# Kernel optimization log

Measured on AMD Instinct MI355X. Metric: run time of the kernel, lower is better.

The kernel has to match this reference:

```python
import jax, jax.numpy as jnp
import numpy as np


def mesa_head(xh, yh, qh, lam):
    # xh = per-head 'inputs' (v_proj output), yh = 'targets' (k_proj output),
    # qh = queries; all [T, d]. lam is this head's scalar lambda.
    T, d = xh.shape
    init_inv = jnp.eye(d, dtype=xh.dtype) * lam

    def step(inv, tok):
        x_t, q_t = tok
        Hx = inv @ x_t                      # [d]   (cur_inverse @ x)
        xH = x_t @ inv                      # [d]   (x^T @ cur_inverse)
        denom = 1.0 + x_t @ Hx              # scalar: forward=1 + x^T H x
        new_inv = inv - jnp.outer(Hx, xH) / denom   # Sherman-Morrison rank-1 update
        return new_inv, new_inv @ q_t       # pred_t = S_t @ q_t

    _, preds = jax.lax.scan(step, init_inv, (xh, qh))  # preds: [T, d]

    # scaled_dot_product_attention(preds, xh, yh) with masked=True,
    # use_softmax=False, normalization=False: tril-masked linear attention.
    logits = preds @ xh.T                               # [T, T]
    mask = jnp.tril(jnp.ones((T, T), dtype=bool))
    logits = jnp.where(mask, logits, jnp.zeros((), dtype=logits.dtype))
    return logits @ yh                                  # [T, d]


def reference(x, Wq, Wk, Wv, Wo, lambdas):
    B, T, E = x.shape
    H = lambdas.shape[0]
    d = Wq.shape[1] // H
    q = (x @ Wq).reshape(B, T, H, d)   # query_heads
    k = (x @ Wk).reshape(B, T, H, d)   # target_heads
    v = (x @ Wv).reshape(B, T, H, d)   # input_heads
    # Original call: mesa(input_heads, target_heads, query_heads, lambdas, norm)
    over_batch = jax.vmap(mesa_head, in_axes=(0, 0, 0, None))
    over_heads = jax.vmap(over_batch, in_axes=(2, 2, 2, 0), out_axes=-1)
    mesa_out = over_heads(v, k, q, lambdas)             # [B, T, d, H]
    # Faithful to original: reshape combines (d, H) in that order before o_proj.
    out = mesa_out.reshape(B, T, H * d) @ Wo            # [B, T, E]
    return out


def setup_inputs() -> dict:
    key = jax.random.key(0)
    ks = jax.random.split(key, 6)
    B, T, E, H, d = 2, 1024, 512, 8, 64
    s_in = 1.0 / np.sqrt(E).astype(np.float32)
    s_out = 1.0 / np.sqrt(H * d).astype(np.float32)
    return {
        "x": jax.random.normal(ks[0], (B, T, E), dtype=jnp.float32),
        "Wq": jax.random.normal(ks[1], (E, H * d), dtype=jnp.float32) * s_in,
        "Wk": jax.random.normal(ks[2], (E, H * d), dtype=jnp.float32) * s_in,
        "Wv": jax.random.normal(ks[3], (E, H * d), dtype=jnp.float32) * s_in,
        "Wo": jax.random.normal(ks[4], (H * d, E), dtype=jnp.float32) * s_out,
        "lambdas": jnp.ones((H,), dtype=jnp.float32),
    }
```

## Files before the change

### kernel.cpp

```cpp
#include <hip/hip_runtime.h>

#define T_SEQ 1024
#define DH 64
#define NH 8
#define NB 2
#define EMB 512
#define CS 32
#define NCH 32
#define ACH 16
#define NCHAIN 16

typedef __attribute__((ext_vector_type(8))) short bf16x8;
typedef __attribute__((ext_vector_type(4))) float f32x4;

__device__ __forceinline__ int swz4(int r, int c4) {
    return r * 16 + ((c4 ^ (r >> 2)) & 15);
}

__device__ __forceinline__ void fma4(float4& o, float s, const float4& b) {
    o.x += s * b.x; o.y += s * b.y; o.z += s * b.z; o.w += s * b.w;
}

__device__ __forceinline__ ushort f2bf(float f) {
    unsigned u = __float_as_uint(f);
    return (ushort)((u + 0x7FFFu + ((u >> 16) & 1u)) >> 16);
}
__device__ __forceinline__ float bf2f(ushort h) {
    return __uint_as_float(((unsigned)h) << 16);
}
__device__ __forceinline__ void split2(float f, ushort& hi, ushort& lo) {
    hi = f2bf(f);
    lo = f2bf(f - bf2f(hi));
}

__global__ __launch_bounds__(256) void prep_qkv(
    const float* __restrict__ x, const float* __restrict__ W0,
    const float* __restrict__ W1, const float* __restrict__ W2,
    ushort* __restrict__ x_hi, ushort* __restrict__ x_lo,
    ushort* __restrict__ Wt_hi, ushort* __restrict__ Wt_lo) {
    int zz = blockIdx.z;
    int t = threadIdx.x;
    __shared__ float T[64][65];
    if (zz < 3) {
        const float* W = (zz == 0) ? W0 : (zz == 1) ? W1 : W2;
        ushort* hi = Wt_hi + (size_t)zz * 262144;
        ushort* lo = Wt_lo + (size_t)zz * 262144;
        int kk0 = blockIdx.x * 64, n0 = blockIdx.y * 64;
#pragma unroll
        for (int i = 0; i < 4; ++i) {
            int rl = i * 16 + (t >> 4);
            float4 vv = *(const float4*)&W[(size_t)(kk0 + rl) * 512 + n0 + (t & 15) * 4];
            T[rl][(t & 15) * 4 + 0] = vv.x;
            T[rl][(t & 15) * 4 + 1] = vv.y;
            T[rl][(t & 15) * 4 + 2] = vv.z;
            T[rl][(t & 15) * 4 + 3] = vv.w;
        }
        __syncthreads();
        int nl = t >> 2, kl = (t & 3) * 16;
#pragma unroll
        for (int j4 = 0; j4 < 4; ++j4) {
            ushort4 h4, l4;
            split2(T[kl + j4 * 4 + 0][nl], h4.x, l4.x);
            split2(T[kl + j4 * 4 + 1][nl], h4.y, l4.y);
            split2(T[kl + j4 * 4 + 2][nl], h4.z, l4.z);
            split2(T[kl + j4 * 4 + 3][nl], h4.w, l4.w);
            size_t dst = (size_t)(n0 + nl) * 512 + kk0 + kl + j4 * 4;
            *(ushort4*)&hi[dst] = h4;
            *(ushort4*)&lo[dst] = l4;
        }
    } else {
        int bid = blockIdx.y * 8 + blockIdx.x;
        const float4* in = (const float4*)x;
        ushort4* hi = (ushort4*)x_hi;
        ushort4* lo = (ushort4*)x_lo;
#pragma unroll
        for (int i = 0; i < 16; ++i) {
            int id = (bid * 16 + i) * 256 + t;
            float4 xv = in[id];
            ushort4 h, l;
            split2(xv.x, h.x, l.x);
            split2(xv.y, h.y, l.y);
            split2(xv.z, h.z, l.z);
            split2(xv.w, h.w, l.w);
            hi[id] = h;
            lo[id] = l;
        }
    }
}

template <int MODE>
__global__ __launch_bounds__(256) void mfma_gemm(
    const ushort* __restrict__ Ahi, const ushort* __restrict__ Alo,
    const ushort* __restrict__ Bth, const ushort* __restrict__ Btl,
    float* __restrict__ o0, float* __restrict__ o1, float* __restrict__ o2) {
    int bm = blockIdx.x, bn = blockIdx.y, zz = blockIdx.z;
    const ushort* Bh = Bth + (size_t)zz * 262144;
    const ushort* Bl = Btl + (size_t)zz * 262144;
    float* out = (MODE == 0) ? ((zz == 0) ? o0 : (zz == 1) ? o1 : o2) : o0;

    __shared__ ushort Ash[128 * 40];
    __shared__ ushort Asl[128 * 40];
    __shared__ ushort Bsh[64 * 40];
    __shared__ ushort Bsl[64 * 40];

    int tid = threadIdx.x;
    int lane = tid & 63, wid = tid >> 6;
    int wm = wid >> 1, wn = wid & 1;
    int fr = lane & 15, fk = (lane >> 4) * 8;
    int sr = tid >> 2, sc = (tid & 3) * 8;

    f32x4 zero = {0.f, 0.f, 0.f, 0.f};
    f32x4 acc[4][2];
#pragma unroll
    for (int f = 0; f < 4; ++f)
#pragma unroll
        for (int g = 0; g < 2; ++g) acc[f][g] = zero;

    const ushort* gAh = Ahi + (size_t)(bm * 128 + sr) * 512 + sc;
    const ushort* gAl = Alo + (size_t)(bm * 128 + sr) * 512 + sc;
    const ushort* gBh = Bh + (size_t)(bn * 64 + sr) * 512 + sc;
    const ushort* gBl = Bl + (size_t)(bn * 64 + sr) * 512 + sc;

    for (int k0 = 0; k0 < 512; k0 += 32) {
        uint4 a0 = *(const uint4*)(gAh + k0);
        uint4 a1 = *(const uint4*)(gAh + 64 * 512 + k0);
        uint4 a2 = *(const uint4*)(gAl + k0);
        uint4 a3 = *(const uint4*)(gAl + 64 * 512 + k0);
        uint4 b0 = *(const uint4*)(gBh + k0);
        uint4 b1 = *(const uint4*)(gBl + k0);
        __syncthreads();
        *(uint4*)&Ash[sr * 40 + sc] = a0;
        *(uint4*)&Ash[(sr + 64) * 40 + sc] = a1;
        *(uint4*)&Asl[sr * 40 + sc] = a2;
        *(uint4*)&Asl[(sr + 64) * 40 + sc] = a3;
        *(uint4*)&Bsh[sr * 40 + sc] = b0;
        *(uint4*)&Bsl[sr * 40 + sc] = b1;
        __syncthreads();
        bf16x8 ah[4], al[4], bh[2], blo[2];
#pragma unroll
        for (int f = 0; f < 4; ++f) {
            int r = wm * 64 + f * 16 + fr;
            ah[f] = *(const bf16x8*)&Ash[r * 40 + fk];
            al[f] = *(const bf16x8*)&Asl[r * 40 + fk];
        }
#pragma unroll
        for (int g = 0; g < 2; ++g) {
            int r = wn * 32 + g * 16 + fr;
            bh[g] = *(const bf16x8*)&Bsh[r * 40 + fk];
            blo[g] = *(const bf16x8*)&Bsl[r * 40 + fk];
        }
#pragma unroll
        for (int f = 0; f < 4; ++f)
#pragma unroll
            for (int g = 0; g < 2; ++g) {
                acc[f][g] = __builtin_amdgcn_mfma_f32_16x16x32_bf16(
                    ah[f], bh[g], acc[f][g], 0, 0, 0);
                acc[f][g] = __builtin_amdgcn_mfma_f32_16x16x32_bf16(
                    ah[f], blo[g], acc[f][g], 0, 0, 0);
                acc[f][g] = __builtin_amdgcn_mfma_f32_16x16x32_bf16(
                    al[f], bh[g], acc[f][g], 0, 0, 0);
            }
    }

    int rbase = (lane >> 4) * 4;
#pragma unroll
    for (int f = 0; f < 4; ++f)
#pragma unroll
        for (int g = 0; g < 2; ++g)
#pragma unroll
            for (int j = 0; j < 4; ++j) {
                int m = bm * 128 + wm * 64 + f * 16 + rbase + j;
                int n = bn * 64 + wn * 32 + g * 16 + (lane & 15);
                float val = acc[f][g][j];
                if (MODE == 0) {
                    int b = m >> 10, tt = m & 1023;
                    int h = n >> 6, d = n & 63;
                    out[(((size_t)(b * 8 + h) * 1024 + tt) << 6) + d] = val;
                } else {
                    out[(size_t)m * 512 + n] = val;
                }
            }
}

__global__ __launch_bounds__(256) void gram_kernel(
    const float* __restrict__ v, float* __restrict__ g) {
    int chain = blockIdx.x, chunk = blockIdx.y;
    const float* X = v + ((size_t)chain * T_SEQ + chunk * CS) * DH;
    __shared__ float Xs[CS * 64];
    int tid = threadIdx.x;
#pragma unroll
    for (int i = 0; i < (CS * 16) / 256; ++i)
        ((float4*)Xs)[i * 256 + tid] = ((const float4*)X)[i * 256 + tid];
    __syncthreads();

    int tx = tid & 15, ty = tid >> 4;
    float acc[4][4];
#pragma unroll
    for (int i = 0; i < 4; ++i)
#pragma unroll
        for (int j = 0; j < 4; ++j) acc[i][j] = 0.f;

#pragma unroll 4
    for (int t = 0; t < CS; ++t) {
        float a_[4], b_[4];
#pragma unroll
        for (int i = 0; i < 4; ++i) a_[i] = Xs[t * 64 + ty * 4 + i];
#pragma unroll
        for (int j = 0; j < 4; ++j) b_[j] = Xs[t * 64 + tx * 4 + j];
#pragma unroll
        for (int i = 0; i < 4; ++i)
#pragma unroll
            for (int j = 0; j < 4; ++j) acc[i][j] += a_[i] * b_[j];
    }

    float* gp = g + ((size_t)chain * NCH + chunk) * 4096;
#pragma unroll
    for (int i = 0; i < 4; ++i)
        *(float4*)(gp + (ty * 4 + i) * 64 + tx * 4) =
            make_float4(acc[i][0], acc[i][1], acc[i][2], acc[i][3]);
}

__global__ __launch_bounds__(256) void prefix_kernel(float* __restrict__ g) {
    int gid = blockIdx.x * 256 + threadIdx.x;
    int chain = gid >> 12, elem = gid & 4095;
    float* p = g + (size_t)chain * NCH * 4096 + elem;
    float vals[NCH];
#pragma unroll
    for (int c = 0; c < NCH; ++c) vals[c] = p[(size_t)c * 4096];
    float run = 0.f;
#pragma unroll
    for (int c = 0; c < NCH; ++c) {
        float t = vals[c];
        vals[c] = run;
        run += t;
    }
#pragma unroll
    for (int c = 0; c < NCH; ++c) p[(size_t)c * 4096] = vals[c];
}

__global__ __launch_bounds__(256) void invscan(
    const float* __restrict__ g, const float* __restrict__ v,
    const float* __restrict__ q, const float* __restrict__ lambdas,
    float* __restrict__ preds) {
    int blk = blockIdx.x;
    int chain = blk >> 5, chunk = blk & 31;
    int tid = threadIdx.x;
    int row = tid >> 2, ch = tid & 3, wav = tid >> 6;
    float lam = lambdas[chain & (NH - 1)];

    __shared__ float rbuf[2][64];
    __shared__ float sbuf[2][64];
    __shared__ float Xs[CS * 64];
    __shared__ float Qs[CS * 64];
    __shared__ float Po[CS * 64];
    __shared__ float red[2][6][4];

    float m[16];
    {
        const float4* gp = (const float4*)(g + ((size_t)chain * NCH + chunk) * 4096);
#pragma unroll
        for (int i = 0; i < 4; ++i) {
            float4 t4 = gp[row * 16 + ch * 4 + i];
            m[i * 4 + 0] = t4.x; m[i * 4 + 1] = t4.y;
            m[i * 4 + 2] = t4.z; m[i * 4 + 3] = t4.w;
        }
    }
#pragma unroll
    for (int i = 0; i < 16; ++i)
        if (ch * 16 + i == row) m[i] += lam;

    const float4* vb = (const float4*)(v + ((size_t)chain * T_SEQ + chunk * CS) * DH);
    const float4* qb = (const float4*)(q + ((size_t)chain * T_SEQ + chunk * CS) * DH);
    ((float4*)Xs)[tid] = vb[tid];
    ((float4*)Xs)[256 + tid] = vb[256 + tid];
    ((float4*)Qs)[tid] = qb[tid];
    ((float4*)Qs)[256 + tid] = qb[256 + tid];

    if (row == 0) {
#pragma unroll
        for (int i = 0; i < 4; ++i)
            ((float4*)rbuf[0])[ch * 4 + i] =
                make_float4(m[i * 4], m[i * 4 + 1], m[i * 4 + 2], m[i * 4 + 3]);
    }
    if (row == 1) {
#pragma unroll
        for (int i = 0; i < 4; ++i)
            ((float4*)sbuf[0])[ch * 4 + i] =
                make_float4(m[i * 4], m[i * 4 + 1], m[i * 4 + 2], m[i * 4 + 3]);
    }
    __syncthreads();

#pragma unroll
    for (int pp = 0; pp < 32; ++pp) {
        const int p = 2 * pp;
        const float* rb = rbuf[pp & 1];
        const float* sb = sbuf[pp & 1];
        float r_[16], s_[16];
#pragma unroll
        for (int i = 0; i < 4; ++i) {
            float4 t4 = ((const float4*)rb)[ch * 4 + i];
            r_[i * 4] = t4.x; r_[i * 4 + 1] = t4.y;
            r_[i * 4 + 2] = t4.z; r_[i * 4 + 3] = t4.w;
            float4 u4 = ((const float4*)sb)[ch * 4 + i];
            s_[i * 4] = u4.x; s_[i * 4 + 1] = u4.y;
            s_[i * 4 + 2] = u4.z; s_[i * 4 + 3] = u4.w;
        }
        float rp = rb[p], rp2 = rb[p + 1], sp2 = sb[p + 1];
        float gr = rb[row], gs = sb[row];
        float i1 = 1.f / rp;
        float al = rp2 * i1;
        float i2 = 1.f / (sp2 - al * rp2);
        float c0, ca, cb;
        if (row == p) {
            c0 = 0.f; ca = i1 + al * al * i2; cb = -al * i2;
        } else if (row == p + 1) {
            c0 = 0.f; ca = -al * i2; cb = i2;
        } else {
            float b2 = (gs - al * gr) * i2;
            c0 = 1.f; ca = al * b2 - gr * i1; cb = -b2;
        }
#pragma unroll
        for (int i = 0; i < 16; ++i) m[i] = c0 * m[i] + ca * r_[i] + cb * s_[i];
        if (ch == (p >> 4)) {
            m[p & 15] = -ca;
            m[(p & 15) + 1] = -cb;
        }
        if (pp < 31) {
            if (row == p + 2) {
#pragma unroll
                for (int i = 0; i < 4; ++i)
                    ((float4*)rbuf[(pp + 1) & 1])[ch * 4 + i] =
                        make_float4(m[i * 4], m[i * 4 + 1], m[i * 4 + 2], m[i * 4 + 3]);
            }
            if (row == p + 3) {
#pragma unroll
                for (int i = 0; i < 4; ++i)
                    ((float4*)sbuf[(pp + 1) & 1])[ch * 4 + i] =
                        make_float4(m[i * 4], m[i * 4 + 1], m[i * 4 + 2], m[i * 4 + 3]);
            }
        }
        __syncthreads();
    }

#pragma unroll
    for (int tp = 0; tp < 16; ++tp) {
        const int ta = 2 * tp, tb2 = 2 * tp + 1;
        const int par = tp & 1;
        float pu = 0.f, pw = 0.f, pza = 0.f, pzb = 0.f;
#pragma unroll
        for (int i = 0; i < 4; ++i) {
            float4 xa = ((const float4*)(Xs + ta * 64))[ch * 4 + i];
            float4 xb = ((const float4*)(Xs + tb2 * 64))[ch * 4 + i];
            float4 qa = ((const float4*)(Qs + ta * 64))[ch * 4 + i];
            float4 q4 = ((const float4*)(Qs + tb2 * 64))[ch * 4 + i];
            pu += m[i * 4] * xa.x + m[i * 4 + 1] * xa.y + m[i * 4 + 2] * xa.z + m[i * 4 + 3] * xa.w;
            pw += m[i * 4] * xb.x + m[i * 4 + 1] * xb.y + m[i * 4 + 2] * xb.z + m[i * 4 + 3] * xb.w;
            pza += m[i * 4] * qa.x + m[i * 4 + 1] * qa.y + m[i * 4 + 2] * qa.z + m[i * 4 + 3] * qa.w;
            pzb += m[i * 4] * q4.x + m[i * 4 + 1] * q4.y + m[i * 4 + 2] * q4.z + m[i * 4 + 3] * q4.w;
        }
        pu += __shfl_xor(pu, 1); pu += __shfl_xor(pu, 2);
        pw += __shfl_xor(pw, 1); pw += __shfl_xor(pw, 2);
        pza += __shfl_xor(pza, 1); pza += __shfl_xor(pza, 2);
        pzb += __shfl_xor(pzb, 1); pzb += __shfl_xor(pzb, 2);
        float u = -pu, w = -pw, za = -pza, zb = -pzb;
        if (ch == 0) rbuf[par][row] = u;
        if (ch == 1) sbuf[par][row] = w;
        float a_ = Xs[ta * 64 + row], b_ = Xs[tb2 * 64 + row];
        float qa_ = Qs[ta * 64 + row], qb_ = Qs[tb2 * 64 + row];
        float d0 = a_ * u, d1 = b_ * u, d2 = b_ * w;
        float d3 = qa_ * u, d4 = qb_ * u, d5 = qb_ * w;
#pragma unroll
        for (int off = 32; off; off >>= 1) {
            d0 += __shfl_xor(d0, off); d1 += __shfl_xor(d1, off);
            d2 += __shfl_xor(d2, off); d3 += __shfl_xor(d3, off);
            d4 += __shfl_xor(d4, off); d5 += __shfl_xor(d5, off);
        }
        if ((tid & 63) == 0) {
            red[par][0][wav] = d0; red[par][1][wav] = d1; red[par][2][wav] = d2;
            red[par][3][wav] = d3; red[par][4][wav] = d4; red[par][5][wav] = d5;
        }
        __syncthreads();
        float saa = 0.25f * (red[par][0][0] + red[par][0][1] + red[par][0][2] + red[par][0][3]);
        float sab = 0.25f * (red[par][1][0] + red[par][1][1] + red[par][1][2] + red[par][1][3]);
        float sbb = 0.25f * (red[par][2][0] + red[par][2][1] + red[par][2][2] + red[par][2][3]);
        float c1  = 0.25f * (red[par][3][0] + red[par][3][1] + red[par][3][2] + red[par][3][3]);
        float c2  = 0.25f * (red[par][4][0] + red[par][4][1] + red[par][4][2] + red[par][4][3]);
        float c3  = 0.25f * (red[par][5][0] + red[par][5][1] + red[par][5][2] + red[par][5][3]);
        float k1 = 1.f / (1.f + saa);
        float al2 = sab * k1;
        float k2 = 1.f / (1.f + sbb - sab * al2);
        float vr = w - al2 * u;
        if (ch == 0) Po[ta * 64 + row] = za - (c1 * k1) * u;
        if (ch == 1) Po[tb2 * 64 + row] = zb - (c2 * k1) * u - (k2 * (c3 - al2 * c2)) * vr;
        float cu = k1 * u - al2 * k2 * vr;
        float cw = k2 * vr;
#pragma unroll
        for (int i = 0; i < 4; ++i) {
            float4 uj = ((const float4*)rbuf[par])[ch * 4 + i];
            float4 wj = ((const float4*)sbuf[par])[ch * 4 + i];
            m[i * 4 + 0] += cu * uj.x + cw * wj.x;
            m[i * 4 + 1] += cu * uj.y + cw * wj.y;
            m[i * 4 + 2] += cu * uj.z + cw * wj.z;
            m[i * 4 + 3] += cu * uj.w + cw * wj.w;
        }
    }
    __syncthreads();

    float4* po4 = (float4*)(preds + ((size_t)chain * T_SEQ + chunk * CS) * DH);
    po4[tid] = ((const float4*)Po)[tid];
    po4[256 + tid] = ((const float4*)Po)[256 + tid];
}

__global__ __launch_bounds__(256) void kvg_wot(
    const float* __restrict__ V, const float* __restrict__ Kv,
    float* __restrict__ D, const float* __restrict__ Wo,
    ushort* __restrict__ Wot_hi, ushort* __restrict__ Wot_lo) {
    __shared__ float smem[8192];
    int tid = threadIdx.x;
    if (blockIdx.y < 16) {
        int chain = blockIdx.x, ck = blockIdx.y;
        float* Vs = smem;
        float* Ks2 = smem + 4096;
        const float4* Vb = (const float4*)(V + ((size_t)chain * T_SEQ + ck * 64) * DH);
        const float4* Kb = (const float4*)(Kv + ((size_t)chain * T_SEQ + ck * 64) * DH);
#pragma unroll
        for (int i = 0; i < 4; ++i) {
            ((float4*)Vs)[i * 256 + tid] = Vb[i * 256 + tid];
            ((float4*)Ks2)[i * 256 + tid] = Kb[i * 256 + tid];
        }
        __syncthreads();

        int tx = tid & 15, ty = tid >> 4;
        float acc[4][4];
#pragma unroll
        for (int i = 0; i < 4; ++i)
#pragma unroll
            for (int j = 0; j < 4; ++j) acc[i][j] = 0.f;

#pragma unroll 4
        for (int t = 0; t < 64; ++t) {
            float a_[4], b_[4];
#pragma unroll
            for (int i = 0; i < 4; ++i) a_[i] = Vs[t * 64 + ty * 4 + i];
#pragma unroll
            for (int j = 0; j < 4; ++j) b_[j] = Ks2[t * 64 + tx * 4 + j];
#pragma unroll
            for (int i = 0; i < 4; ++i)
#pragma unroll
                for (int j = 0; j < 4; ++j) acc[i][j] += a_[i] * b_[j];
        }

        float* dp = D + ((size_t)chain * ACH + ck) * 4096;
#pragma unroll
        for (int i = 0; i < 4; ++i)
            *(float4*)(dp + (ty * 4 + i) * 64 + tx * 4) =
                make_float4(acc[i][0], acc[i][1], acc[i][2], acc[i][3]);
    } else {
        int wb = blockIdx.x * 4 + (blockIdx.y - 16);
        int kk0 = (wb >> 3) * 64, n0 = (wb & 7) * 64;
#pragma unroll
        for (int i = 0; i < 4; ++i) {
            int rl = i * 16 + (tid >> 4);
            int rs = rl * 8 + (kk0 >> 6);
            float4 vv = *(const float4*)&Wo[(size_t)rs * 512 + n0 + (tid & 15) * 4];
            smem[rl * 65 + (tid & 15) * 4 + 0] = vv.x;
            smem[rl * 65 + (tid & 15) * 4 + 1] = vv.y;
            smem[rl * 65 + (tid & 15) * 4 + 2] = vv.z;
            smem[rl * 65 + (tid & 15) * 4 + 3] = vv.w;
        }
        __syncthreads();
        int nl = tid >> 2, kl = (tid & 3) * 16;
#pragma unroll
        for (int j4 = 0; j4 < 4; ++j4) {
            ushort4 h4, l4;
            split2(smem[(kl + j4 * 4 + 0) * 65 + nl], h4.x, l4.x);
            split2(smem[(kl + j4 * 4 + 1) * 65 + nl], h4.y, l4.y);
            split2(smem[(kl + j4 * 4 + 2) * 65 + nl], h4.z, l4.z);
            split2(smem[(kl + j4 * 4 + 3) * 65 + nl], h4.w, l4.w);
            size_t dst = (size_t)(n0 + nl) * 512 + kk0 + kl + j4 * 4;
            *(ushort4*)&Wot_hi[dst] = h4;
            *(ushort4*)&Wot_lo[dst] = l4;
        }
    }
}

__global__ __launch_bounds__(256) void kv_prefix(float* __restrict__ d) {
    int gid = blockIdx.x * 256 + threadIdx.x;
    int chain = gid >> 12, elem = gid & 4095;
    float* p = d + (size_t)chain * ACH * 4096 + elem;
    float vals[ACH];
#pragma unroll
    for (int c = 0; c < ACH; ++c) vals[c] = p[(size_t)c * 4096];
    float run = 0.f;
#pragma unroll
    for (int c = 0; c < ACH; ++c) {
        float t = vals[c];
        vals[c] = run;
        run += t;
    }
#pragma unroll
    for (int c = 0; c < ACH; ++c) p[(size_t)c * 4096] = vals[c];
}

__global__ __launch_bounds__(256) void attn_chunk(
    const float* __restrict__ P, const float* __restrict__ V,
    const float* __restrict__ Kv, const float* __restrict__ C,
    ushort* __restrict__ A2_hi, ushort* __restrict__ A2_lo) {
    int ck = blockIdx.x, bh = blockIdx.y;
    int tid = threadIdx.x, tx = tid & 15, ty = tid >> 4;

    __shared__ float4 Ps[64 * 16];
    __shared__ float4 Bs[64 * 16];
    __shared__ float4 Ks[64 * 16];

    int lr = tid >> 2, lc = tid & 3;
    const float4* Pb = (const float4*)(P + ((size_t)bh * T_SEQ + ck * 64) * DH);
    const float4* Vb = (const float4*)(V + ((size_t)bh * T_SEQ + ck * 64) * DH);
    const float4* Kb = (const float4*)(Kv + ((size_t)bh * T_SEQ + ck * 64) * DH);
    const float4* Cb = (const float4*)(C + ((size_t)bh * ACH + ck) * 4096);
#pragma unroll
    for (int i = 0; i < 4; ++i) {
        Ps[swz4(lr, lc + i * 4)] = Pb[lr * 16 + lc + i * 4];
        Bs[swz4(lr, lc + i * 4)] = Cb[lr * 16 + lc + i * 4];
        Ks[swz4(lr, lc + i * 4)] = Kb[lr * 16 + lc + i * 4];
    }

    float4 o[4];
    o[0] = o[1] = o[2] = o[3] = make_float4(0.f, 0.f, 0.f, 0.f);
    __syncthreads();

    const float* Pf = (const float*)Ps;
#pragma unroll 4
    for (int j = 0; j < 64; ++j) {
        float4 b4 = Bs[swz4(j, tx)];
#pragma unroll
        for (int i = 0; i < 4; ++i) {
            float s = Pf[swz4(ty * 4 + i, j >> 2) * 4 + (j & 3)];
            fma4(o[i], s, b4);
        }
    }
    __syncthreads();

#pragma unroll
    for (int i = 0; i < 4; ++i)
        Bs[swz4(lr, lc + i * 4)] = Vb[lr * 16 + lc + i * 4];
    __syncthreads();

    float4 sa[4][4];
#pragma unroll
    for (int i = 0; i < 4; ++i)
#pragma unroll
        for (int j = 0; j < 4; ++j) sa[i][j] = make_float4(0.f, 0.f, 0.f, 0.f);
#pragma unroll
    for (int d4 = 0; d4 < 16; ++d4) {
        float4 a[4], b[4];
#pragma unroll
        for (int i = 0; i < 4; ++i) a[i] = Ps[swz4(ty * 4 + i, d4)];
#pragma unroll
        for (int j = 0; j < 4; ++j) b[j] = Bs[swz4(tx * 4 + j, d4)];
#pragma unroll
        for (int i = 0; i < 4; ++i)
#pragma unroll
            for (int j = 0; j < 4; ++j) {
                sa[i][j].x += a[i].x * b[j].x;
                sa[i][j].y += a[i].y * b[j].y;
                sa[i][j].z += a[i].z * b[j].z;
                sa[i][j].w += a[i].w * b[j].w;
            }
    }
    __syncthreads();

#pragma unroll
    for (int i = 0; i < 4; ++i) {
        int m = ty * 4 + i;
        float sv[4];
#pragma unroll
        for (int j = 0; j < 4; ++j) {
            float s = sa[i][j].x + sa[i][j].y + sa[i][j].z + sa[i][j].w;
            if ((tx * 4 + j) > m) s = 0.f;
            sv[j] = s;
        }
        Bs[swz4(m, tx)] = make_float4(sv[0], sv[1], sv[2], sv[3]);
    }
    __syncthreads();

    const float* Sf = (const float*)Bs;
#pragma unroll 4
    for (int j = 0; j < 64; ++j) {
        float4 b4 = Ks[swz4(j, tx)];
#pragma unroll
        for (int i = 0; i < 4; ++i) {
            float s = Sf[swz4(ty * 4 + i, j >> 2) * 4 + (j & 3)];
            fma4(o[i], s, b4);
        }
    }

    int kkb = ((bh & 7) << 6) + tx * 4;
#pragma unroll
    for (int i = 0; i < 4; ++i) {
        int t = ck * 64 + ty * 4 + i;
        size_t mrow = (size_t)((bh >> 3) << 10) + t;
        ushort4 h, l;
        split2(o[i].x, h.x, l.x);
        split2(o[i].y, h.y, l.y);
        split2(o[i].z, h.z, l.z);
        split2(o[i].w, h.w, l.w);
        *(ushort4*)&A2_hi[mrow * 512 + kkb] = h;
        *(ushort4*)&A2_lo[mrow * 512 + kkb] = l;
    }
}

extern "C" void kernel_launch(void* const* d_in, const int* in_sizes, int n_in,
                              void* d_out, int out_size, void* d_ws, size_t ws_size,
                              hipStream_t stream) {
    const float* x = (const float*)d_in[0];
    const float* Wq = (const float*)d_in[1];
    const float* Wk = (const float*)d_in[2];
    const float* Wv = (const float*)d_in[3];
    const float* Wo = (const float*)d_in[4];
    const float* lambdas = (const float*)d_in[5];
    float* out = (float*)d_out;

    float* ws = (float*)d_ws;
    const size_t SZ = (size_t)NB * NH * T_SEQ * DH;
    float* q = ws;
    float* k = ws + SZ;
    float* v = ws + 2 * SZ;
    float* preds = ws + 3 * SZ;
    ushort* x_hi = (ushort*)(ws + 3 * SZ);
    ushort* x_lo = (ushort*)(ws + 3 * SZ + SZ / 2);
    float* g = ws + 4 * SZ;
    ushort* Wt_hi = (ushort*)(ws + 4 * SZ);
    ushort* Wt_lo = (ushort*)(ws + 4 * SZ + 393216);
    float* dbuf = g;
    ushort* A2_hi = (ushort*)(ws + 5 * SZ);
    ushort* A2_lo = (ushort*)(ws + 5 * SZ + SZ / 2);
    ushort* Wot_hi = (ushort*)ws;
    ushort* Wot_lo = (ushort*)(ws + 131072);

    prep_qkv<<<dim3(8, 8, 4), 256, 0, stream>>>(x, Wq, Wk, Wv,
                                                x_hi, x_lo, Wt_hi, Wt_lo);
    mfma_gemm<0><<<dim3(16, 8, 3), 256, 0, stream>>>(
        x_hi, x_lo, Wt_hi, Wt_lo, q, k, v);
    gram_kernel<<<dim3(NCHAIN, NCH), 256, 0, stream>>>(v, g);
    prefix_kernel<<<dim3(256), 256, 0, stream>>>(g);
    invscan<<<dim3(NCHAIN * NCH), 256, 0, stream>>>(g, v, q, lambdas, preds);
    kvg_wot<<<dim3(NCHAIN, ACH + 4), 256, 0, stream>>>(v, k, dbuf, Wo,
                                                       Wot_hi, Wot_lo);
    kv_prefix<<<dim3(256), 256, 0, stream>>>(dbuf);
    attn_chunk<<<dim3(ACH, NCHAIN), 256, 0, stream>>>(preds, v, k, dbuf,
                                                      A2_hi, A2_lo);
    mfma_gemm<1><<<dim3(16, 8, 1), 256, 0, stream>>>(
        A2_hi, A2_lo, Wot_hi, Wot_lo, out, out, out);
}
```

Before: 129.0 us.

## Replace sequential in-chunk rank-2 updates with block Cholesky solve

In the invscan kernel, the per-token sequential Sherman-Morrison updates inside each 32-token chunk are replaced by a blocked formulation. All chunk-start products H·x and H·q are computed first. A 32x32 Gram matrix (I + U^T X) and a cross matrix (U^T Q) are formed, the Gram matrix is Cholesky factored by a single 32-thread wave, and masked triangular solves produce the corrections applied to the predictions. This removes the 16 per-pair block-wide barriers and reductions, and pads shared arrays to cut bank conflicts. In exchange it adds a serial Cholesky and triangular solves run by few threads, and the numerics change.

```diff
diff --git a/kernel.cpp b/kernel.cpp
--- a/kernel.cpp
+++ b/kernel.cpp
@@ -9,6 +9,7 @@
 #define NCH 32
 #define ACH 16
 #define NCHAIN 16
+#define PF 68
 
 typedef __attribute__((ext_vector_type(8))) short bf16x8;
 typedef __attribute__((ext_vector_type(4))) float f32x4;
@@ -245,15 +246,19 @@
     int blk = blockIdx.x;
     int chain = blk >> 5, chunk = blk & 31;
     int tid = threadIdx.x;
-    int row = tid >> 2, ch = tid & 3, wav = tid >> 6;
+    int row = tid >> 2, ch = tid & 3;
     float lam = lambdas[chain & (NH - 1)];
 
     __shared__ float rbuf[2][64];
     __shared__ float sbuf[2][64];
-    __shared__ float Xs[CS * 64];
-    __shared__ float Qs[CS * 64];
-    __shared__ float Po[CS * 64];
-    __shared__ float red[2][6][4];
+    __shared__ float Xs[CS * PF];
+    __shared__ float Qs[CS * PF];
+    __shared__ float Ul[CS * PF];
+    __shared__ float P0l[CS * PF];
+    __shared__ float Ga[32 * 33];
+    __shared__ float Cc[32 * 33];
+    __shared__ float Ww[32 * 33];
+    __shared__ float Zz[32 * 33];
 
     float m[16];
     {
@@ -271,10 +276,13 @@
 
     const float4* vb = (const float4*)(v + ((size_t)chain * T_SEQ + chunk * CS) * DH);
     const float4* qb = (const float4*)(q + ((size_t)chain * T_SEQ + chunk * CS) * DH);
-    ((float4*)Xs)[tid] = vb[tid];
-    ((float4*)Xs)[256 + tid] = vb[256 + tid];
-    ((float4*)Qs)[tid] = qb[tid];
-    ((float4*)Qs)[256 + tid] = qb[256 + tid];
+    {
+        int f0 = tid, f1 = 256 + tid;
+        ((float4*)Xs)[(f0 >> 4) * 17 + (f0 & 15)] = vb[f0];
+        ((float4*)Xs)[(f1 >> 4) * 17 + (f1 & 15)] = vb[f1];
+        ((float4*)Qs)[(f0 >> 4) * 17 + (f0 & 15)] = qb[f0];
+        ((float4*)Qs)[(f1 >> 4) * 17 + (f1 & 15)] = qb[f1];
+    }
 
     if (row == 0) {
 #pragma unroll
@@ -342,73 +350,117 @@
         __syncthreads();
     }
 
-#pragma unroll
-    for (int tp = 0; tp < 16; ++tp) {
-        const int ta = 2 * tp, tb2 = 2 * tp + 1;
-        const int par = tp & 1;
-        float pu = 0.f, pw = 0.f, pza = 0.f, pzb = 0.f;
+    for (int t = 0; t < CS; ++t) {
+        const float4* xt = (const float4*)(Xs + t * PF);
+        const float4* qt = (const float4*)(Qs + t * PF);
+        float hx = 0.f, hq = 0.f;
 #pragma unroll
         for (int i = 0; i < 4; ++i) {
-            float4 xa = ((const float4*)(Xs + ta * 64))[ch * 4 + i];
-            float4 xb = ((const float4*)(Xs + tb2 * 64))[ch * 4 + i];
-            float4 qa = ((const float4*)(Qs + ta * 64))[ch * 4 + i];
-            float4 q4 = ((const float4*)(Qs + tb2 * 64))[ch * 4 + i];
-            pu += m[i * 4] * xa.x + m[i * 4 + 1] * xa.y + m[i * 4 + 2] * xa.z + m[i * 4 + 3] * xa.w;
-            pw += m[i * 4] * xb.x + m[i * 4 + 1] * xb.y + m[i * 4 + 2] * xb.z + m[i * 4 + 3] * xb.w;
-            pza += m[i * 4] * qa.x + m[i * 4 + 1] * qa.y + m[i * 4 + 2] * qa.z + m[i * 4 + 3] * qa.w;
-            pzb += m[i * 4] * q4.x + m[i * 4 + 1] * q4.y + m[i * 4 + 2] * q4.z + m[i * 4 + 3] * q4.w;
-        }
-        pu += __shfl_xor(pu, 1); pu += __shfl_xor(pu, 2);
-        pw += __shfl_xor(pw, 1); pw += __shfl_xor(pw, 2);
-        pza += __shfl_xor(pza, 1); pza += __shfl_xor(pza, 2);
-        pzb += __shfl_xor(pzb, 1); pzb += __shfl_xor(pzb, 2);
-        float u = -pu, w = -pw, za = -pza, zb = -pzb;
-        if (ch == 0) rbuf[par][row] = u;
-        if (ch == 1) sbuf[par][row] = w;
-        float a_ = Xs[ta * 64 + row], b_ = Xs[tb2 * 64 + row];
-        float qa_ = Qs[ta * 64 + row], qb_ = Qs[tb2 * 64 + row];
-        float d0 = a_ * u, d1 = b_ * u, d2 = b_ * w;
-        float d3 = qa_ * u, d4 = qb_ * u, d5 = qb_ * w;
-#pragma unroll
-        for (int off = 32; off; off >>= 1) {
-            d0 += __shfl_xor(d0, off); d1 += __shfl_xor(d1, off);
-            d2 += __shfl_xor(d2, off); d3 += __shfl_xor(d3, off);
-            d4 += __shfl_xor(d4, off); d5 += __shfl_xor(d5, off);
-        }
-        if ((tid & 63) == 0) {
-            red[par][0][wav] = d0; red[par][1][wav] = d1; red[par][2][wav] = d2;
-            red[par][3][wav] = d3; red[par][4][wav] = d4; red[par][5][wav] = d5;
-        }
-        __syncthreads();
-        float saa = 0.25f * (red[par][0][0] + red[par][0][1] + red[par][0][2] + red[par][0][3]);
-        float sab = 0.25f * (red[par][1][0] + red[par][1][1] + red[par][1][2] + red[par][1][3]);
-        float sbb = 0.25f * (red[par][2][0] + red[par][2][1] + red[par][2][2] + red[par][2][3]);
-        float c1  = 0.25f * (red[par][3][0] + red[par][3][1] + red[par][3][2] + red[par][3][3]);
-        float c2  = 0.25f * (red[par][4][0] + red[par][4][1] + red[par][4][2] + red[par][4][3]);
-        float c3  = 0.25f * (red[par][5][0] + red[par][5][1] + red[par][5][2] + red[par][5][3]);
-        float k1 = 1.f / (1.f + saa);
-        float al2 = sab * k1;
-        float k2 = 1.f / (1.f + sbb - sab * al2);
-        float vr = w - al2 * u;
-        if (ch == 0) Po[ta * 64 + row] = za - (c1 * k1) * u;
-        if (ch == 1) Po[tb2 * 64 + row] = zb - (c2 * k1) * u - (k2 * (c3 - al2 * c2)) * vr;
-        float cu = k1 * u - al2 * k2 * vr;
-        float cw = k2 * vr;
-#pragma unroll
-        for (int i = 0; i < 4; ++i) {
-            float4 uj = ((const float4*)rbuf[par])[ch * 4 + i];
-            float4 wj = ((const float4*)sbuf[par])[ch * 4 + i];
-            m[i * 4 + 0] += cu * uj.x + cw * wj.x;
-            m[i * 4 + 1] += cu * uj.y + cw * wj.y;
-            m[i * 4 + 2] += cu * uj.z + cw * wj.z;
-            m[i * 4 + 3] += cu * uj.w + cw * wj.w;
-        }
-    }
-    __syncthreads();
-
-    float4* po4 = (float4*)(preds + ((size_t)chain * T_SEQ + chunk * CS) * DH);
-    po4[tid] = ((const float4*)Po)[tid];
-    po4[256 + tid] = ((const float4*)Po)[256 + tid];
+            float4 x4 = xt[ch * 4 + i];
+            float4 q4 = qt[ch * 4 + i];
+            hx += m[i * 4] * x4.x + m[i * 4 + 1] * x4.y + m[i * 4 + 2] * x4.z + m[i * 4 + 3] * x4.w;
+            hq += m[i * 4] * q4.x + m[i * 4 + 1] * q4.y + m[i * 4 + 2] * q4.z + m[i * 4 + 3] * q4.w;
+        }
+        hx += __shfl_xor(hx, 1); hx += __shfl_xor(hx, 2);
+        hq += __shfl_xor(hq, 1); hq += __shfl_xor(hq, 2);
+        if (ch == 0) {
+            Ul[t * PF + row] = -hx;
+            P0l[t * PF + row] = -hq;
+        }
+    }
+    __syncthreads();
+
+    {
+        int sid = tid >> 3, tq = tid & 7;
+        float us[64];
+        const float4* up = (const float4*)(Ul + sid * PF);
+#pragma unroll
+        for (int i = 0; i < 16; ++i) {
+            float4 u4 = up[i];
+            us[i * 4] = u4.x; us[i * 4 + 1] = u4.y;
+            us[i * 4 + 2] = u4.z; us[i * 4 + 3] = u4.w;
+        }
+#pragma unroll
+        for (int tt = 0; tt < 4; ++tt) {
+            int t = tq * 4 + tt;
+            const float4* xt = (const float4*)(Xs + t * PF);
+            const float4* qt = (const float4*)(Qs + t * PF);
+            float gg = 0.f, cc = 0.f;
+#pragma unroll
+            for (int i = 0; i < 16; ++i) {
+                float4 x4 = xt[i];
+                float4 q4 = qt[i];
+                gg += us[i * 4] * x4.x + us[i * 4 + 1] * x4.y + us[i * 4 + 2] * x4.z + us[i * 4 + 3] * x4.w;
+                cc += us[i * 4] * q4.x + us[i * 4 + 1] * q4.y + us[i * 4 + 2] * q4.z + us[i * 4 + 3] * q4.w;
+            }
+            Ga[sid * 33 + t] = gg + ((sid == t) ? 1.f : 0.f);
+            Cc[sid * 33 + t] = cc;
+        }
+    }
+    __syncthreads();
+
+    if (tid < 32) {
+        int i = tid;
+        for (int k = 0; k < 32; ++k) {
+            float dk = sqrtf(Ga[k * 33 + k]);
+            float aik = Ga[i * 33 + k] / dk;
+            if (i > k) Ga[i * 33 + k] = aik;
+            if (i == k) Ga[k * 33 + k] = dk;
+            float colik = (i > k) ? aik : 0.f;
+            for (int j = k + 1; j < 32; ++j) {
+                float ljk = Ga[j * 33 + k];
+                if (i >= j) Ga[i * 33 + j] -= colik * ljk;
+            }
+        }
+    }
+    __syncthreads();
+
+    {
+        int col = tid >> 3, r = tid & 7;
+        for (int k = 0; k < 32; ++k) {
+            float part = 0.f;
+            for (int i = r; i < k; i += 8)
+                part += Ga[k * 33 + i] * Ww[i * 33 + col];
+            part += __shfl_xor(part, 1);
+            part += __shfl_xor(part, 2);
+            part += __shfl_xor(part, 4);
+            if (r == 0)
+                Ww[k * 33 + col] = (Cc[k * 33 + col] - part) / Ga[k * 33 + k];
+        }
+        for (int k = 31; k >= 0; --k) {
+            float part = 0.f;
+            for (int i = k + 1 + r; i < 32; i += 8)
+                part += Ga[i * 33 + k] * Zz[i * 33 + col];
+            part += __shfl_xor(part, 1);
+            part += __shfl_xor(part, 2);
+            part += __shfl_xor(part, 4);
+            if (r == 0) {
+                float wt = (k <= col) ? Ww[k * 33 + col] : 0.f;
+                Zz[k * 33 + col] = (wt - part) / Ga[k * 33 + k];
+            }
+        }
+    }
+    __syncthreads();
+
+    {
+        int t = tid >> 3, dq = tid & 7;
+        float4 a0 = make_float4(0.f, 0.f, 0.f, 0.f);
+        float4 a1 = make_float4(0.f, 0.f, 0.f, 0.f);
+        for (int s = 0; s < 32; ++s) {
+            float z = Zz[s * 33 + t];
+            const float4* ur = (const float4*)(Ul + s * PF);
+            float4 u0 = ur[dq * 2], u1 = ur[dq * 2 + 1];
+            fma4(a0, z, u0);
+            fma4(a1, z, u1);
+        }
+        const float4* p0 = (const float4*)(P0l + t * PF);
+        float4 b0 = p0[dq * 2], b1 = p0[dq * 2 + 1];
+        b0.x -= a0.x; b0.y -= a0.y; b0.z -= a0.z; b0.w -= a0.w;
+        b1.x -= a1.x; b1.y -= a1.y; b1.z -= a1.z; b1.w -= a1.w;
+        float* pb = preds + ((size_t)chain * T_SEQ + chunk * CS) * DH;
+        *(float4*)&pb[t * 64 + dq * 8] = b0;
+        *(float4*)&pb[t * 64 + dq * 8 + 4] = b1;
+    }
 }
 
 __global__ __launch_bounds__(256) void kvg_wot(
```

Result: slower. 173.5 us (+34.5%).
